# Performance work log

Measured on AMD Instinct MI355X. Metric: run time of the kernel, lower is better.

Reference implementation:

```python
import jax, jax.numpy as jnp
import numpy as np

NUM_HEADS = 8
D_MODEL = 512
HEAD_DIM = D_MODEL // NUM_HEADS


def _conv1x1(x, W, b):
    # Conv1d(kernel_size=1): x [B, Cin, N], W [Cout, Cin], b [Cout] -> [B, Cout, N]
    return jnp.einsum('oi,bin->bon', W, x) + b[None, :, None]


def setup_inputs() -> dict:
    key = jax.random.key(0)
    ks = jax.random.split(key, 12)
    B, D, N, Mlen = 4, D_MODEL, 2048, 2048
    inp = {
        'query': jax.random.normal(ks[0], (B, D, N), dtype=jnp.float32),
        'key':   jax.random.normal(ks[1], (B, D, Mlen), dtype=jnp.float32),
        'value': jax.random.normal(ks[2], (B, D, Mlen), dtype=jnp.float32),
        'M':     jnp.ones((B, N, Mlen), dtype=jnp.int32),
    }
    scale = 0.02
    inp['Wq'] = jax.random.normal(ks[3], (D, D), dtype=jnp.float32) * scale
    inp['bq'] = jnp.zeros((D,), dtype=jnp.float32)
    inp['Wk'] = jax.random.normal(ks[4], (D, D), dtype=jnp.float32) * scale
    inp['bk'] = jnp.zeros((D,), dtype=jnp.float32)
    inp['Wv'] = jax.random.normal(ks[5], (D, D), dtype=jnp.float32) * scale
    inp['bv'] = jnp.zeros((D,), dtype=jnp.float32)
    inp['Wm'] = jax.random.normal(ks[6], (D, D), dtype=jnp.float32) * scale
    inp['bm'] = jnp.zeros((D,), dtype=jnp.float32)
    return inp


def reference(query, key, value, M, Wq, bq, Wk, bk, Wv, bv, Wm, bm):
    B = query.shape[0]
    # 1x1-conv projections, then channel split as [head_dim, heads] (matches torch .view)
    q = _conv1x1(query, Wq, bq).reshape(B, HEAD_DIM, NUM_HEADS, -1)  # [B, d, h, N]
    k = _conv1x1(key,   Wk, bk).reshape(B, HEAD_DIM, NUM_HEADS, -1)  # [B, d, h, M]
    v = _conv1x1(value, Wv, bv).reshape(B, HEAD_DIM, NUM_HEADS, -1)  # [B, d, h, M]
    scores = jnp.einsum('bdhn,bdhm->bhnm', q, k) / jnp.sqrt(jnp.float32(HEAD_DIM))
    # mask: positions with M==0 are disallowed -> fill with -finfo.max
    bad = (1 - M)[:, None, :, :].astype(bool)  # [B, 1, N, M], broadcasts over heads
    scores = jnp.where(bad, -jnp.finfo(scores.dtype).max, scores)
    prob = jax.nn.softmax(scores, axis=-1)  # [B, h, N, M]
    x = jnp.einsum('bhnm,bdhm->bdhn', prob, v)  # [B, d, h, N]
    out = _conv1x1(x.reshape(B, HEAD_DIM * NUM_HEADS, -1), Wm, bm)  # [B, D, N]
    return out
```

## Files before the change

kernel.cpp:

```cpp
#include <hip/hip_runtime.h>

typedef __attribute__((ext_vector_type(8))) short s8v;
typedef __attribute__((ext_vector_type(4))) float f4v;
typedef unsigned short u16;
typedef unsigned long long u64;

#define DM 512
#define NH 8
#define HD 64
#define BB 4
#define NN 2048

__device__ __forceinline__ float bf2f(u16 x){ return __uint_as_float(((unsigned)x)<<16); }
__device__ __forceinline__ u16 f2bf(float f){
  unsigned u = __float_as_uint(f);
  u += 0x7FFFu + ((u>>16)&1u);
  return (u16)(u>>16);
}
__device__ __forceinline__ void gl2lds16(const u16* g, u16* l){
  __builtin_amdgcn_global_load_lds((__attribute__((address_space(1))) void*)(g),
                                   (__attribute__((address_space(3))) void*)(l), 16, 0, 0);
}

__global__ void k_permute(const float* Wq, const float* bq, const float* Wk, const float* bk,
                          const float* Wv, const float* bv, const float* Wm,
                          u16* Wp, u16* Wmp, float* bp){
  int blk = blockIdx.x, tid = threadIdx.x;
  if (blk < 1536){
    int t = blk >> 9, op = blk & 511;
    int srow = ((op & 63) << 3) | (op >> 6);
    const float* W = (t==0) ? Wq : ((t==1) ? Wk : Wv);
    for (int j = tid; j < 512; j += 256)
      Wp[((size_t)t*512 + op)*512 + j] = f2bf(W[(size_t)srow*512 + j]);
  } else if (blk < 2048){
    int o = blk - 1536;
    for (int c = tid; c < 512; c += 256){
      int scol = ((c & 63) << 3) | (c >> 6);
      Wmp[(size_t)o*512 + c] = f2bf(Wm[(size_t)o*512 + scol]);
    }
  } else {
    for (int idx = tid; idx < 1536; idx += 256){
      int t = idx >> 9, op = idx & 511;
      const float* bs = (t==0) ? bq : ((t==1) ? bk : bv);
      int srow = ((op & 63) << 3) | (op >> 6);
      bp[idx] = bs[srow];
    }
  }
}

__global__ __launch_bounds__(256) void k_transpose(const float* q, const float* k, const float* v, u16* XT){
  __shared__ u16 T[64*72];
  int blk = blockIdx.x, tid = threadIdx.x;
  int rt = blk & 31; blk >>= 5;
  int it = blk & 7;  blk >>= 3;
  int b  = blk & 3;  int t = blk >> 2;
  const float* src = (t==0) ? q : ((t==1) ? k : v);
  src += (size_t)b*DM*NN;
  int i0 = it*64, r0 = rt*64;
  int il = tid>>4, rj = (tid&15)*4;
  #pragma unroll
  for (int p=0;p<4;p++){
    int i = il + p*16;
    float4 vv = *(const float4*)&src[(size_t)(i0+i)*NN + r0 + rj];
    float fv[4] = {vv.x, vv.y, vv.z, vv.w};
    #pragma unroll
    for (int qq=0;qq<4;qq++){
      int r = rj + qq;
      int sr = ((r&3)<<4) | (r>>2);
      T[sr*72 + i] = f2bf(fv[qq]);
    }
  }
  __syncthreads();
  u16* dst = XT + ((size_t)(t*4+b)*NN)*DM;
  int rl = tid>>3, ib = (tid&7)*8;
  #pragma unroll
  for (int p=0;p<2;p++){
    int r = rl + p*32;
    int sr = ((r&3)<<4) | (r>>2);
    s8v vv = *(s8v*)&T[sr*72 + ib];
    *(s8v*)&dst[(size_t)(r0+r)*DM + i0 + ib] = vv;
  }
}

__global__ __launch_bounds__(256) void k_proj(const u16* XT, const u16* Wp, const float* bp,
                                              u16* P, u16* VT){
  __shared__ u16 Al[128*32];
  __shared__ u16 Bl[128*32];
  __shared__ u16 S[128*72];
  int blk = blockIdx.x, tid = threadIdx.x;
  int nt = blk & 3; int mt = blk >> 2;
  int tb = mt >> 4;
  int t  = tb >> 2, b = tb & 3;
  int r0 = (mt & 15)*128, o0 = nt*128;
  const u16* Abase = XT + ((size_t)tb*NN + r0)*DM;
  const u16* Bbase = Wp + ((size_t)t*512 + o0)*DM;

  int w = tid>>6, L = tid&63, li = L&15, lq = L>>4;
  int wr = w>>1, wc = w&1;
  int srow = tid>>2;
  int g8   = ((tid&3) ^ ((tid>>3)&3))*8;
  u16* AldsW = &Al[((tid&192))*8];
  u16* BldsW = &Bl[((tid&192))*8];
  int sw = (li>>1)&3;

  f4v acc[4][4];
  #pragma unroll
  for (int a=0;a<4;a++)
    #pragma unroll
    for (int c2=0;c2<4;c2++) acc[a][c2] = (f4v){0.f,0.f,0.f,0.f};

  for (int kk=0; kk<16; kk++){
    int k0 = kk*32;
    __syncthreads();
    #pragma unroll
    for (int c=0;c<2;c++){
      gl2lds16(&Abase[(size_t)(srow + c*64)*DM + k0 + g8], AldsW + c*2048);
      gl2lds16(&Bbase[(size_t)(srow + c*64)*DM + k0 + g8], BldsW + c*2048);
    }
    __syncthreads();
    s8v af[4], bfr[4];
    #pragma unroll
    for (int a=0;a<4;a++){
      int r = wr*64 + a*16 + li;
      af[a] = *(s8v*)&Al[r*32 + ((lq ^ sw))*8];
    }
    #pragma unroll
    for (int c2=0;c2<4;c2++){
      int r = wc*64 + c2*16 + li;
      bfr[c2] = *(s8v*)&Bl[r*32 + ((lq ^ sw))*8];
    }
    #pragma unroll
    for (int a=0;a<4;a++)
      #pragma unroll
      for (int c2=0;c2<4;c2++)
        acc[a][c2] = __builtin_amdgcn_mfma_f32_16x16x32_bf16(af[a], bfr[c2], acc[a][c2], 0, 0, 0);
  }

  if (t < 2){
    float scale = (t==0) ? 0.125f : 1.0f;
    #pragma unroll
    for (int c2=0;c2<4;c2++){
      int col = wc*64 + c2*16 + li;
      int h = (o0 + col) >> 6, d = col & 63;
      float bias = bp[t*512 + o0 + col];
      u16* Pb = P + (((size_t)tb*NH + h)*NN)*HD + d;
      #pragma unroll
      for (int a=0;a<4;a++){
        #pragma unroll
        for (int ri=0;ri<4;ri++){
          int row = r0 + wr*64 + a*16 + lq*4 + ri;
          Pb[(size_t)row*HD] = f2bf((acc[a][c2][ri] + bias)*scale);
        }
      }
    }
  } else {
    #pragma unroll
    for (int p=0;p<2;p++){
      if (wc == p){
        #pragma unroll
        for (int c2=0;c2<4;c2++){
          int cl = c2*16 + li;
          float bias = bp[2*512 + o0 + p*64 + cl];
          #pragma unroll
          for (int a=0;a<4;a++)
            #pragma unroll
            for (int ri=0;ri<4;ri++)
              S[(wr*64 + a*16 + lq*4 + ri)*72 + cl] = f2bf(acc[a][c2][ri] + bias);
        }
      }
      __syncthreads();
      int dl = tid & 63;
      u16* Vb = VT + (((size_t)b*NH + (o0>>6) + p)*HD + dl)*NN + r0;
      #pragma unroll
      for (int it2=0; it2<4; it2++){
        int mseg = (tid>>6) + it2*4;
        s8v vv; u16* vp = (u16*)&vv;
        #pragma unroll
        for (int j=0;j<8;j++) vp[j] = S[(mseg*8+j)*72 + dl];
        *(s8v*)&Vb[mseg*8] = vv;
      }
      __syncthreads();
    }
  }
}

__global__ void k_maskpack(const int* M, u64* bits){
  int tid = threadIdx.x;
  size_t word = (size_t)blockIdx.x*4 + (tid>>6);
  int lane = tid & 63;
  int v = M[word*64 + lane];
  u64 bal = __ballot(v == 1);
  if (lane == 0) bits[word] = bal;
}

__global__ __launch_bounds__(256) void k_maskand(const u64* bits, u64* allw){
  __shared__ u64 red[256];
  int bnt = blockIdx.x, tid = threadIdx.x;
  int mt = tid & 31, rg = tid >> 5;
  const u64* base = bits + (size_t)bnt*64*32;
  u64 v = ~0ull;
  #pragma unroll
  for (int j=0;j<8;j++) v &= base[(size_t)(rg*8+j)*32 + mt];
  red[tid] = v;
  __syncthreads();
  if (tid < 32){
    u64 a = red[tid];
    #pragma unroll
    for (int g2=1; g2<8; g2++) a &= red[g2*32 + tid];
    allw[(size_t)bnt*32 + tid] = a;
  }
}

__global__ __launch_bounds__(256) void k_flash(const u16* P, const u16* VT, const u64* bits,
                                               const u64* allw, u16* Xout){
  __shared__ u16 Ql[64*72];
  __shared__ u16 Kl[64*72];
  __shared__ u16 Vt[64*72];
  __shared__ u16 Pl[64*72];
  int blk = blockIdx.x, tid = threadIdx.x;
  int nt = blk & 31; int bh = blk >> 5;
  int b = bh >> 3;
  int n0 = nt*64;
  const size_t TSZ = (size_t)BB*NH*NN*HD;
  const u16* Qb = P + ((size_t)bh*NN + n0)*HD;
  const u16* Kb = P + TSZ + (size_t)bh*NN*HD;
  const u16* Vb = VT + (size_t)bh*HD*NN;
  const u64* awp = allw + ((size_t)b*32 + nt)*32;

  int sm = tid>>3, sd = (tid&7)*8;
  int w = tid>>6, L = tid&63, li = L&15, lq = L>>4;
  int sli = ((li&3)<<2) | (li>>2);

  #pragma unroll
  for (int p=0;p<2;p++)
    *(s8v*)&Ql[(sm+p*32)*72 + sd] = *(const s8v*)&Qb[(size_t)(sm+p*32)*HD + sd];

  s8v ones;
  #pragma unroll
  for (int j=0;j<8;j++) ((u16*)&ones)[j] = 0x3F80;

  f4v O[4], RS;
  RS = (f4v){0.f,0.f,0.f,0.f};
  #pragma unroll
  for (int j=0;j<4;j++) O[j] = (f4v){0.f,0.f,0.f,0.f};

  for (int mt=0; mt<32; mt++){
    int m0 = mt*64;
    u64 aw = awp[mt];
    bool fast = (aw == ~0ull);
    s8v kreg[2], vreg[2];
    #pragma unroll
    for (int p=0;p<2;p++){
      kreg[p] = *(const s8v*)&Kb[(size_t)(m0+sm+p*32)*HD + sd];
      vreg[p] = *(const s8v*)&Vb[(size_t)(sm+p*32)*NN + m0 + sd];
    }
    __syncthreads();
    #pragma unroll
    for (int p=0;p<2;p++){
      *(s8v*)&Kl[(sm+p*32)*72 + sd] = kreg[p];
      *(s8v*)&Vt[(sm+p*32)*72 + sd] = vreg[p];
    }
    __syncthreads();

    s8v a0 = *(s8v*)&Ql[(w*16+li)*72 + lq*8];
    s8v a1 = *(s8v*)&Ql[(w*16+li)*72 + 32 + lq*8];
    f4v S[4];
    #pragma unroll
    for (int j=0;j<4;j++){
      s8v b0 = *(s8v*)&Kl[(j*16+li)*72 + lq*8];
      s8v b1 = *(s8v*)&Kl[(j*16+li)*72 + 32 + lq*8];
      f4v c = (f4v){0.f,0.f,0.f,0.f};
      c = __builtin_amdgcn_mfma_f32_16x16x32_bf16(a0, b0, c, 0, 0, 0);
      c = __builtin_amdgcn_mfma_f32_16x16x32_bf16(a1, b1, c, 0, 0, 0);
      S[j] = c;
    }

    if (fast){
      #pragma unroll
      for (int ri=0;ri<4;ri++){
        int srow = (w*16 + ((ri&3)<<2) + lq)*72;
        #pragma unroll
        for (int j=0;j<4;j++){
          unsigned u = __float_as_uint(__expf(S[j][ri])) + 0x8000u;
          Pl[srow + j*16 + li] = (u16)(u>>16);
        }
      }
    } else {
      u64 mw[4];
      #pragma unroll
      for (int ri=0;ri<4;ri++)
        mw[ri] = bits[((size_t)b*NN + n0 + w*16 + lq*4 + ri)*32 + mt];
      #pragma unroll
      for (int ri=0;ri<4;ri++){
        int srow = (w*16 + ((ri&3)<<2) + lq)*72;
        #pragma unroll
        for (int j=0;j<4;j++){
          float e = __expf(S[j][ri]);
          e = ((mw[ri]>>(j*16+li)) & 1ull) ? e : 0.f;
          unsigned u = __float_as_uint(e) + 0x8000u;
          Pl[srow + j*16 + li] = (u16)(u>>16);
        }
      }
    }

    s8v ap0 = *(s8v*)&Pl[(w*16+sli)*72 + lq*8];
    s8v ap1 = *(s8v*)&Pl[(w*16+sli)*72 + 32 + lq*8];
    RS = __builtin_amdgcn_mfma_f32_16x16x32_bf16(ap0, ones, RS, 0, 0, 0);
    RS = __builtin_amdgcn_mfma_f32_16x16x32_bf16(ap1, ones, RS, 0, 0, 0);
    #pragma unroll
    for (int j2=0;j2<4;j2++){
      s8v b0 = *(s8v*)&Vt[(j2*16+li)*72 + lq*8];
      s8v b1 = *(s8v*)&Vt[(j2*16+li)*72 + 32 + lq*8];
      O[j2] = __builtin_amdgcn_mfma_f32_16x16x32_bf16(ap0, b0, O[j2], 0, 0, 0);
      O[j2] = __builtin_amdgcn_mfma_f32_16x16x32_bf16(ap1, b1, O[j2], 0, 0, 0);
    }
  }

  float inv[4];
  #pragma unroll
  for (int ri=0;ri<4;ri++) inv[ri] = (RS[ri] > 0.f) ? 1.0f/RS[ri] : 0.f;
  int h = bh & 7;
  u16* Xo = Xout + ((size_t)b*NN)*DM + h*HD;
  #pragma unroll
  for (int j2=0;j2<4;j2++){
    int d = j2*16 + li;
    #pragma unroll
    for (int ri=0;ri<4;ri++){
      int n = n0 + w*16 + lq*4 + ri;
      Xo[(size_t)n*DM + d] = f2bf(O[j2][ri]*inv[ri]);
    }
  }
}

__global__ __launch_bounds__(256) void k_out(const u16* Wmp, const u16* Xout, const float* bm, float* out){
  __shared__ u16 Al[128*32];
  __shared__ u16 Bl[128*32];
  int blk = blockIdx.x, tid = threadIdx.x;
  int nt = blk & 15; blk >>= 4;
  int ot = blk & 3;  int b = blk >> 2;
  int o0 = ot*128, n0 = nt*128;
  const u16* Abase = Wmp + (size_t)o0*DM;
  const u16* Bbase = Xout + ((size_t)b*NN + n0)*DM;

  int w = tid>>6, L = tid&63, li = L&15, lq = L>>4;
  int wr = w>>1, wc = w&1;
  int srow = tid>>2;
  int g8   = ((tid&3) ^ ((tid>>3)&3))*8;
  u16* AldsW = &Al[((tid&192))*8];
  u16* BldsW = &Bl[((tid&192))*8];
  int sw = (li>>1)&3;

  f4v acc[4][4];
  #pragma unroll
  for (int a=0;a<4;a++)
    #pragma unroll
    for (int c2=0;c2<4;c2++) acc[a][c2] = (f4v){0.f,0.f,0.f,0.f};

  for (int kk=0; kk<16; kk++){
    int k0 = kk*32;
    __syncthreads();
    #pragma unroll
    for (int c=0;c<2;c++){
      gl2lds16(&Abase[(size_t)(srow + c*64)*DM + k0 + g8], AldsW + c*2048);
      gl2lds16(&Bbase[(size_t)(srow + c*64)*DM + k0 + g8], BldsW + c*2048);
    }
    __syncthreads();
    s8v af[4], bfr[4];
    #pragma unroll
    for (int a=0;a<4;a++){
      int r = wr*64 + a*16 + li;
      af[a] = *(s8v*)&Al[r*32 + ((lq ^ sw))*8];
    }
    #pragma unroll
    for (int c2=0;c2<4;c2++){
      int r = wc*64 + c2*16 + li;
      bfr[c2] = *(s8v*)&Bl[r*32 + ((lq ^ sw))*8];
    }
    #pragma unroll
    for (int a=0;a<4;a++)
      #pragma unroll
      for (int c2=0;c2<4;c2++)
        acc[a][c2] = __builtin_amdgcn_mfma_f32_16x16x32_bf16(af[a], bfr[c2], acc[a][c2], 0, 0, 0);
  }

  #pragma unroll
  for (int a=0;a<4;a++){
    #pragma unroll
    for (int ri=0;ri<4;ri++){
      int o = o0 + wr*64 + a*16 + lq*4 + ri;
      float bias = bm[o];
      float* ob = out + ((size_t)b*DM + o)*NN + n0 + wc*64;
      #pragma unroll
      for (int c2=0;c2<4;c2++)
        ob[c2*16 + li] = acc[a][c2][ri] + bias;
    }
  }
}

extern "C" void kernel_launch(void* const* d_in, const int* in_sizes, int n_in,
                              void* d_out, int out_size, void* d_ws, size_t ws_size,
                              hipStream_t stream){
  const float* q  = (const float*)d_in[0];
  const float* k  = (const float*)d_in[1];
  const float* v  = (const float*)d_in[2];
  const int*   M  = (const int*)d_in[3];
  const float* Wq = (const float*)d_in[4];
  const float* bq = (const float*)d_in[5];
  const float* Wk = (const float*)d_in[6];
  const float* bk = (const float*)d_in[7];
  const float* Wv = (const float*)d_in[8];
  const float* bv = (const float*)d_in[9];
  const float* Wm = (const float*)d_in[10];
  const float* bm = (const float*)d_in[11];

  char* ws = (char*)d_ws;
  u16*   XT   = (u16*)(ws + 0);
  u16*   P    = (u16*)(ws + 25165824);
  u16*   VT   = (u16*)(ws + 41943040);
  u16*   Wp   = (u16*)(ws + 50331648);
  u16*   Wmp  = (u16*)(ws + 51904512);
  float* bp   = (float*)(ws + 52428800);
  u64*   bits = (u64*)(ws + 52434944);
  u16*   Xout = (u16*)(ws + 54532096);
  u64*   allw = (u64*)(ws + 62920704);
  float* out  = (float*)d_out;

  k_permute<<<2049, 256, 0, stream>>>(Wq, bq, Wk, bk, Wv, bv, Wm, Wp, Wmp, bp);
  k_transpose<<<3072, 256, 0, stream>>>(q, k, v, XT);
  k_proj<<<768, 256, 0, stream>>>(XT, Wp, bp, P, VT);
  k_maskpack<<<65536, 256, 0, stream>>>(M, bits);
  k_maskand<<<128, 256, 0, stream>>>(bits, allw);
  k_flash<<<1024, 256, 0, stream>>>(P, VT, bits, allw, Xout);
  k_out<<<256, 256, 0, stream>>>(Wmp, Xout, bm, out);
}
```

Baseline: 317.5 us.

## Keep P in registers via transposed S and split key dim across waves

The flash kernel now computes S transposed (K as the A operand, Q fragments kept in registers) so each wave owns a 16-key slice for all 64 queries. The exponentials are packed directly into fp16 MFMA operands with no LDS round trip for P, and V is stored as fp16 to match the 16x16x16 f16 MFMA. Row sums are accumulated in registers, and the per-wave partial O tiles are reduced through shared memory at the end, with vectorized output stores. This removes the P shared-memory write/read and the ones-MFMA row sum. In exchange it uses 64 accumulator floats per lane, a serialized 4-phase cross-wave reduction, and fp16 range limits on V and the unnormalized exp values.

```diff
diff --git a/kernel.cpp b/kernel.cpp
--- a/kernel.cpp
+++ b/kernel.cpp
@@ -2,6 +2,7 @@
 
 typedef __attribute__((ext_vector_type(8))) short s8v;
 typedef __attribute__((ext_vector_type(4))) float f4v;
+typedef _Float16 h4 __attribute__((ext_vector_type(4)));
 typedef unsigned short u16;
 typedef unsigned long long u64;
 
@@ -164,8 +165,10 @@
           #pragma unroll
           for (int a=0;a<4;a++)
             #pragma unroll
-            for (int ri=0;ri<4;ri++)
-              S[(wr*64 + a*16 + lq*4 + ri)*72 + cl] = f2bf(acc[a][c2][ri] + bias);
+            for (int ri=0;ri<4;ri++){
+              _Float16 hh = (_Float16)(acc[a][c2][ri] + bias);
+              S[(wr*64 + a*16 + lq*4 + ri)*72 + cl] = *(const u16*)&hh;
+            }
         }
       }
       __syncthreads();
@@ -211,38 +214,40 @@
   }
 }
 
-__global__ __launch_bounds__(256) void k_flash(const u16* P, const u16* VT, const u64* bits,
+__global__ __launch_bounds__(256) void k_flash(const u16* Pq, const u16* VT, const u64* bits,
                                                const u64* allw, u16* Xout){
-  __shared__ u16 Ql[64*72];
-  __shared__ u16 Kl[64*72];
-  __shared__ u16 Vt[64*72];
-  __shared__ u16 Pl[64*72];
+  __shared__ __align__(16) char smem[19456];
+  u16*   Kl  = (u16*)smem;
+  u16*   Vl  = (u16*)(smem + 9216);
+  float* Red = (float*)smem;
+  float* lsb = (float*)(smem + 18432);
+
   int blk = blockIdx.x, tid = threadIdx.x;
   int nt = blk & 31; int bh = blk >> 5;
   int b = bh >> 3;
   int n0 = nt*64;
   const size_t TSZ = (size_t)BB*NH*NN*HD;
-  const u16* Qb = P + ((size_t)bh*NN + n0)*HD;
-  const u16* Kb = P + TSZ + (size_t)bh*NN*HD;
+  const u16* Qb = Pq + ((size_t)bh*NN + n0)*HD;
+  const u16* Kb = Pq + TSZ + (size_t)bh*NN*HD;
   const u16* Vb = VT + (size_t)bh*HD*NN;
   const u64* awp = allw + ((size_t)b*32 + nt)*32;
 
   int sm = tid>>3, sd = (tid&7)*8;
   int w = tid>>6, L = tid&63, li = L&15, lq = L>>4;
-  int sli = ((li&3)<<2) | (li>>2);
-
-  #pragma unroll
-  for (int p=0;p<2;p++)
-    *(s8v*)&Ql[(sm+p*32)*72 + sd] = *(const s8v*)&Qb[(size_t)(sm+p*32)*HD + sd];
-
-  s8v ones;
-  #pragma unroll
-  for (int j=0;j<8;j++) ((u16*)&ones)[j] = 0x3F80;
-
-  f4v O[4], RS;
-  RS = (f4v){0.f,0.f,0.f,0.f};
-  #pragma unroll
-  for (int j=0;j<4;j++) O[j] = (f4v){0.f,0.f,0.f,0.f};
+
+  s8v Qf[4][2];
+  #pragma unroll
+  for (int j=0;j<4;j++)
+    #pragma unroll
+    for (int h2=0;h2<2;h2++)
+      Qf[j][h2] = *(const s8v*)&Qb[(size_t)(j*16+li)*HD + h2*32 + lq*8];
+
+  f4v O[4][4];
+  #pragma unroll
+  for (int j2=0;j2<4;j2++)
+    #pragma unroll
+    for (int j=0;j<4;j++) O[j2][j] = (f4v){0.f,0.f,0.f,0.f};
+  float ls[4] = {0.f,0.f,0.f,0.f};
 
   for (int mt=0; mt<32; mt++){
     int m0 = mt*64;
@@ -258,78 +263,98 @@
     #pragma unroll
     for (int p=0;p<2;p++){
       *(s8v*)&Kl[(sm+p*32)*72 + sd] = kreg[p];
-      *(s8v*)&Vt[(sm+p*32)*72 + sd] = vreg[p];
-    }
-    __syncthreads();
-
-    s8v a0 = *(s8v*)&Ql[(w*16+li)*72 + lq*8];
-    s8v a1 = *(s8v*)&Ql[(w*16+li)*72 + 32 + lq*8];
+      *(s8v*)&Vl[(sm+p*32)*72 + sd] = vreg[p];
+    }
+    __syncthreads();
+
+    s8v Kf0 = *(s8v*)&Kl[(w*16+li)*72 + lq*8];
+    s8v Kf1 = *(s8v*)&Kl[(w*16+li)*72 + 32 + lq*8];
+
     f4v S[4];
     #pragma unroll
     for (int j=0;j<4;j++){
-      s8v b0 = *(s8v*)&Kl[(j*16+li)*72 + lq*8];
-      s8v b1 = *(s8v*)&Kl[(j*16+li)*72 + 32 + lq*8];
       f4v c = (f4v){0.f,0.f,0.f,0.f};
-      c = __builtin_amdgcn_mfma_f32_16x16x32_bf16(a0, b0, c, 0, 0, 0);
-      c = __builtin_amdgcn_mfma_f32_16x16x32_bf16(a1, b1, c, 0, 0, 0);
+      c = __builtin_amdgcn_mfma_f32_16x16x32_bf16(Kf0, Qf[j][0], c, 0, 0, 0);
+      c = __builtin_amdgcn_mfma_f32_16x16x32_bf16(Kf1, Qf[j][1], c, 0, 0, 0);
       S[j] = c;
     }
 
+    h4 Pf[4];
     if (fast){
       #pragma unroll
-      for (int ri=0;ri<4;ri++){
-        int srow = (w*16 + ((ri&3)<<2) + lq)*72;
-        #pragma unroll
-        for (int j=0;j<4;j++){
-          unsigned u = __float_as_uint(__expf(S[j][ri])) + 0x8000u;
-          Pl[srow + j*16 + li] = (u16)(u>>16);
-        }
+      for (int j=0;j<4;j++){
+        float e0 = __expf(S[j][0]), e1 = __expf(S[j][1]);
+        float e2 = __expf(S[j][2]), e3 = __expf(S[j][3]);
+        ls[j] += (e0+e1)+(e2+e3);
+        Pf[j][0] = (_Float16)e0; Pf[j][1] = (_Float16)e1;
+        Pf[j][2] = (_Float16)e2; Pf[j][3] = (_Float16)e3;
       }
     } else {
-      u64 mw[4];
-      #pragma unroll
-      for (int ri=0;ri<4;ri++)
-        mw[ri] = bits[((size_t)b*NN + n0 + w*16 + lq*4 + ri)*32 + mt];
-      #pragma unroll
-      for (int ri=0;ri<4;ri++){
-        int srow = (w*16 + ((ri&3)<<2) + lq)*72;
+      int mbit = w*16 + lq*4;
+      #pragma unroll
+      for (int j=0;j<4;j++){
+        u64 mw = bits[((size_t)b*NN + n0 + j*16 + li)*32 + mt];
+        float e[4];
         #pragma unroll
-        for (int j=0;j<4;j++){
-          float e = __expf(S[j][ri]);
-          e = ((mw[ri]>>(j*16+li)) & 1ull) ? e : 0.f;
-          unsigned u = __float_as_uint(e) + 0x8000u;
-          Pl[srow + j*16 + li] = (u16)(u>>16);
+        for (int r=0;r<4;r++){
+          float ev = __expf(S[j][r]);
+          e[r] = ((mw>>(mbit+r)) & 1ull) ? ev : 0.f;
+          Pf[j][r] = (_Float16)e[r];
         }
+        ls[j] += (e[0]+e[1])+(e[2]+e[3]);
       }
     }
 
-    s8v ap0 = *(s8v*)&Pl[(w*16+sli)*72 + lq*8];
-    s8v ap1 = *(s8v*)&Pl[(w*16+sli)*72 + 32 + lq*8];
-    RS = __builtin_amdgcn_mfma_f32_16x16x32_bf16(ap0, ones, RS, 0, 0, 0);
-    RS = __builtin_amdgcn_mfma_f32_16x16x32_bf16(ap1, ones, RS, 0, 0, 0);
     #pragma unroll
     for (int j2=0;j2<4;j2++){
-      s8v b0 = *(s8v*)&Vt[(j2*16+li)*72 + lq*8];
-      s8v b1 = *(s8v*)&Vt[(j2*16+li)*72 + 32 + lq*8];
-      O[j2] = __builtin_amdgcn_mfma_f32_16x16x32_bf16(ap0, b0, O[j2], 0, 0, 0);
-      O[j2] = __builtin_amdgcn_mfma_f32_16x16x32_bf16(ap1, b1, O[j2], 0, 0, 0);
-    }
-  }
-
-  float inv[4];
-  #pragma unroll
-  for (int ri=0;ri<4;ri++) inv[ri] = (RS[ri] > 0.f) ? 1.0f/RS[ri] : 0.f;
+      h4 Vf = *(h4*)&Vl[(j2*16+li)*72 + w*16 + lq*4];
+      #pragma unroll
+      for (int j=0;j<4;j++)
+        O[j2][j] = __builtin_amdgcn_mfma_f32_16x16x16f16(Vf, Pf[j], O[j2][j], 0, 0, 0);
+    }
+  }
+
+  #pragma unroll
+  for (int j=0;j<4;j++){
+    float r = ls[j];
+    r += __shfl_xor(r, 16); r += __shfl_xor(r, 32);
+    ls[j] = r;
+  }
+  if (lq == 0){
+    #pragma unroll
+    for (int j=0;j<4;j++) lsb[w*64 + j*16 + li] = ls[j];
+  }
+  __syncthreads();
+
+  #pragma unroll
+  for (int ph=0; ph<4; ph++){
+    if (w == ph){
+      #pragma unroll
+      for (int j=0;j<4;j++)
+        #pragma unroll
+        for (int j2=0;j2<4;j2++){
+          f4v* p = (f4v*)&Red[(j*16+li)*68 + j2*16 + lq*4];
+          if (ph == 0) *p = O[j2][j];
+          else { f4v t = *p; t += O[j2][j]; *p = t; }
+        }
+    }
+    __syncthreads();
+  }
+
+  int n = tid>>2, d0 = (tid&3)*16;
+  float s = lsb[n] + lsb[64+n] + lsb[128+n] + lsb[192+n];
+  float inv = (s > 0.f) ? 1.0f/s : 0.f;
   int h = bh & 7;
-  u16* Xo = Xout + ((size_t)b*NN)*DM + h*HD;
-  #pragma unroll
-  for (int j2=0;j2<4;j2++){
-    int d = j2*16 + li;
-    #pragma unroll
-    for (int ri=0;ri<4;ri++){
-      int n = n0 + w*16 + lq*4 + ri;
-      Xo[(size_t)n*DM + d] = f2bf(O[j2][ri]*inv[ri]);
-    }
-  }
+  u16* Xo = Xout + ((size_t)b*NN + n0 + n)*DM + h*HD + d0;
+  u16 tmp[16];
+  #pragma unroll
+  for (int e2=0;e2<4;e2++){
+    f4v vv = *(f4v*)&Red[n*68 + d0 + e2*4];
+    #pragma unroll
+    for (int q2=0;q2<4;q2++) tmp[e2*4+q2] = f2bf(vv[q2]*inv);
+  }
+  *(s8v*)&Xo[0] = *(s8v*)&tmp[0];
+  *(s8v*)&Xo[8] = *(s8v*)&tmp[8];
 }
 
 __global__ __launch_bounds__(256) void k_out(const u16* Wmp, const u16* Xout, const float* bm, float* out){
```

Result: faster. 299.2 us (-5.8%).
